# Optimization experiments

Measured on AMD Instinct MI355X. Metric: run time of the kernel, lower is better.

## Reference

```python
import jax, jax.numpy as jnp
import numpy as np

B, S, D = 2, 2048, 2048
H = 32
HD = D // H  # 64
EPS = 1e-4


def setup_inputs() -> dict:
    key = jax.random.key(0)
    ks = jax.random.split(key, 9)
    hidden_states = jax.random.normal(ks[0], (B, S, D), dtype=jnp.float32)
    # multiplicative causal mask
    attention_mask = jnp.tril(jnp.ones((S, S), dtype=jnp.float32))[None, None]
    scale = 0.02
    wq = jax.random.normal(ks[1], (D, D), dtype=jnp.float32) * scale
    wk = jax.random.normal(ks[2], (D, D), dtype=jnp.float32) * scale
    wv = jax.random.normal(ks[3], (D, D), dtype=jnp.float32) * scale
    wo = jax.random.normal(ks[4], (D, D), dtype=jnp.float32) * scale
    bq = jax.random.normal(ks[5], (D,), dtype=jnp.float32) * scale
    bk = jax.random.normal(ks[6], (D,), dtype=jnp.float32) * scale
    bv = jax.random.normal(ks[7], (D,), dtype=jnp.float32) * scale
    bo = jax.random.normal(ks[8], (D,), dtype=jnp.float32) * scale
    return {"hidden_states": hidden_states, "attention_mask": attention_mask,
            "wq": wq, "bq": bq, "wk": wk, "bk": bk, "wv": wv, "bv": bv,
            "wo": wo, "bo": bo}


def _split_heads(x):
    # [B, S, D] -> [B, H, S, HD]
    b, s, _ = x.shape
    return x.reshape(b, s, H, HD).transpose(0, 2, 1, 3)


def reference(hidden_states, attention_mask, wq, bq, wk, bk, wv, bv, wo, bo):
    scaling = HD ** -0.5
    q = (hidden_states @ wq.T + bq) * scaling
    k = hidden_states @ wk.T + bk
    v = hidden_states @ wv.T + bv
    q, k, v = _split_heads(q), _split_heads(k), _split_heads(v)
    # ELU+1 feature map, then sum-normalize over head dim
    q = jax.nn.elu(q) + 1.0
    k = jax.nn.elu(k) + 1.0
    q = q / (q.sum(-1, keepdims=True) + EPS)
    k = k / (k.sum(-1, keepdims=True) + EPS)
    # quadratic attention: [B, H, S, S]
    attn = jnp.einsum('bhsd,bhtd->bhst', q, k) * (HD ** -0.5)
    attn = attn * attention_mask  # multiplicative mask
    out = jnp.einsum('bhst,bhtd->bhsd', attn, v)  # [B, H, S, HD]
    out = out.transpose(0, 2, 1, 3).reshape(hidden_states.shape[0], -1, D)
    return out @ wo.T + bo
```

## Files before the change

kernel.cpp:

```cpp
#include <hip/hip_runtime.h>

typedef __bf16 bf16x8 __attribute__((ext_vector_type(8)));
typedef float f32x4 __attribute__((ext_vector_type(4)));

#define GLDS(g, l) __builtin_amdgcn_global_load_lds(                              \
    (const __attribute__((address_space(1))) void*)(g),                            \
    (__attribute__((address_space(3))) void*)(l), 16, 0, 0)

__device__ __forceinline__ unsigned short f2bf(float f) {
  unsigned int u = __builtin_bit_cast(unsigned int, f);
  u = (u + 0x7fffu + ((u >> 16) & 1u)) >> 16;
  return (unsigned short)u;
}
__device__ __forceinline__ float bf2f(unsigned short h) {
  unsigned int u = ((unsigned int)h) << 16;
  return __builtin_bit_cast(float, u);
}

__global__ __launch_bounds__(256) void cvt_f32_bf16(
    const float* __restrict__ in, unsigned short* __restrict__ out, int n4) {
  int i = blockIdx.x * 256 + threadIdx.x;
  if (i < n4) {
    float4 v = ((const float4*)in)[i];
    ushort4 o;
    o.x = f2bf(v.x); o.y = f2bf(v.y); o.z = f2bf(v.z); o.w = f2bf(v.w);
    ((ushort4*)out)[i] = o;
  }
}

__global__ __launch_bounds__(256) void cvt_w4(
    const float* __restrict__ w0, const float* __restrict__ w1,
    const float* __restrict__ w2, const float* __restrict__ w3,
    unsigned short* __restrict__ out) {
  const int y = blockIdx.y;
  const float* src = (y == 0) ? w0 : (y == 1) ? w1 : (y == 2) ? w2 : w3;
  const int i = blockIdx.x * 256 + threadIdx.x;
  float4 v = ((const float4*)src)[i];
  ushort4 o;
  o.x = f2bf(v.x); o.y = f2bf(v.y); o.z = f2bf(v.z); o.w = f2bf(v.w);
  ((ushort4*)(out + (size_t)y * 4194304))[i] = o;
}

__global__ __launch_bounds__(512, 2) void gemm256_qkv(
    const unsigned short* __restrict__ A, const unsigned short* __restrict__ Bw,
    const float* __restrict__ bq, const float* __restrict__ bk, const float* __restrict__ bv,
    unsigned short* __restrict__ oQ, unsigned short* __restrict__ oK,
    unsigned short* __restrict__ oV) {
  constexpr int K = 2048, NT = 32;
  __shared__ unsigned short lds[81920];
  const int tid = threadIdx.x, lane = tid & 63, wid = tid >> 6;
  const int wm = wid >> 2, wn = wid & 3;

  const int g0 = blockIdx.x;
  const int wg = (g0 & 7) * 48 + (g0 >> 3);
  const int l = wg % 96, chunk = wg / 96;
  const int bx = chunk * 6 + l / 16;
  const int by = l % 16;

  const int rloc = tid >> 3;
  const size_t gcoff = (size_t)(((lane & 7) ^ (lane >> 3)) << 3);
  const unsigned short* gA[4];
  const unsigned short* gB[4];
#pragma unroll
  for (int c = 0; c < 4; ++c) {
    gA[c] = A  + (size_t)(by * 256 + c * 64 + rloc) * K + gcoff;
    gB[c] = Bw + (size_t)(bx * 256 + c * 64 + rloc) * K + gcoff;
  }

#define ABu(b) ((b) * 16384)
#define BBu(b) (49152 + (b) * 16384)
#define STAGE_A(c, b) GLDS(gA[c], lds + ABu(b) + (c) * 4096 + wid * 512)
#define STAGE_B(c, b) GLDS(gB[c], lds + BBu(b) + (c) * 4096 + wid * 512)

  const int arow = (wm * 128 + (lane & 15)) * 64;
  const int brow = (wn * 64 + (lane & 15)) * 64;
  const int sw0 = (((lane >> 4)) ^ (lane & 7)) << 3;
  const int sw1 = ((4 + (lane >> 4)) ^ (lane & 7)) << 3;

  f32x4 acc[8][4] = {};

#pragma unroll
  for (int c = 0; c < 4; ++c) STAGE_A(c, 0);
#pragma unroll
  for (int c = 0; c < 4; ++c) gA[c] += 64;
#pragma unroll
  for (int c = 0; c < 4; ++c) STAGE_B(c, 0);
#pragma unroll
  for (int c = 0; c < 4; ++c) gB[c] += 64;
#pragma unroll
  for (int c = 0; c < 4; ++c) STAGE_A(c, 1);
#pragma unroll
  for (int c = 0; c < 4; ++c) gA[c] += 64;
  asm volatile("s_waitcnt vmcnt(4)" ::: "memory");
  __builtin_amdgcn_s_barrier();

  for (int t = 0; t < NT; ++t) {
    const int Ab = ABu(t % 3) + arow;
    const int Bb = BBu(t & 1) + brow;
    const int Asb = (t + 2) % 3, Bsb = (t + 1) & 1;
    const bool stA = (t + 2 < NT), stB = (t + 1 < NT);
    bf16x8 Af[4], Bf[4];

    if (stB) { STAGE_B(0, Bsb); STAGE_B(1, Bsb); }
#pragma unroll
    for (int n = 0; n < 4; ++n) Bf[n] = *(const bf16x8*)&lds[Bb + n * 1024 + sw0];
#pragma unroll
    for (int m = 0; m < 4; ++m) Af[m] = *(const bf16x8*)&lds[Ab + m * 1024 + sw0];
    __builtin_amdgcn_s_barrier();
    __builtin_amdgcn_s_setprio(1);
#pragma unroll
    for (int m = 0; m < 4; ++m)
#pragma unroll
      for (int n = 0; n < 4; ++n)
        acc[m][n] = __builtin_amdgcn_mfma_f32_16x16x32_bf16(Af[m], Bf[n], acc[m][n], 0, 0, 0);
    __builtin_amdgcn_s_setprio(0);
    __builtin_amdgcn_s_barrier();

    if (stB) {
      STAGE_B(2, Bsb); STAGE_B(3, Bsb);
#pragma unroll
      for (int c = 0; c < 4; ++c) gB[c] += 64;
    }
#pragma unroll
    for (int m = 0; m < 4; ++m) Af[m] = *(const bf16x8*)&lds[Ab + (m + 4) * 1024 + sw0];
    __builtin_amdgcn_s_barrier();
    __builtin_amdgcn_s_setprio(1);
#pragma unroll
    for (int m = 0; m < 4; ++m)
#pragma unroll
      for (int n = 0; n < 4; ++n)
        acc[m + 4][n] = __builtin_amdgcn_mfma_f32_16x16x32_bf16(Af[m], Bf[n], acc[m + 4][n], 0, 0, 0);
    __builtin_amdgcn_s_setprio(0);
    __builtin_amdgcn_s_barrier();

    if (stA) { STAGE_A(0, Asb); STAGE_A(1, Asb); }
#pragma unroll
    for (int n = 0; n < 4; ++n) Bf[n] = *(const bf16x8*)&lds[Bb + n * 1024 + sw1];
#pragma unroll
    for (int m = 0; m < 4; ++m) Af[m] = *(const bf16x8*)&lds[Ab + m * 1024 + sw1];
    __builtin_amdgcn_s_barrier();
    __builtin_amdgcn_s_setprio(1);
#pragma unroll
    for (int m = 0; m < 4; ++m)
#pragma unroll
      for (int n = 0; n < 4; ++n)
        acc[m][n] = __builtin_amdgcn_mfma_f32_16x16x32_bf16(Af[m], Bf[n], acc[m][n], 0, 0, 0);
    __builtin_amdgcn_s_setprio(0);
    __builtin_amdgcn_s_barrier();

    if (stA) {
      STAGE_A(2, Asb); STAGE_A(3, Asb);
#pragma unroll
      for (int c = 0; c < 4; ++c) gA[c] += 64;
    }
#pragma unroll
    for (int m = 0; m < 4; ++m) Af[m] = *(const bf16x8*)&lds[Ab + (m + 4) * 1024 + sw1];
    __builtin_amdgcn_s_barrier();
    __builtin_amdgcn_s_setprio(1);
#pragma unroll
    for (int m = 0; m < 4; ++m)
#pragma unroll
      for (int n = 0; n < 4; ++n)
        acc[m + 4][n] = __builtin_amdgcn_mfma_f32_16x16x32_bf16(Af[m], Bf[n], acc[m + 4][n], 0, 0, 0);
    __builtin_amdgcn_s_setprio(0);
    if (stA)      asm volatile("s_waitcnt vmcnt(4)" ::: "memory");
    else if (stB) asm volatile("s_waitcnt vmcnt(0)" ::: "memory");
    __builtin_amdgcn_s_barrier();
  }

  const int head = bx * 4 + wn;
  const int type = head >> 5;
  const int h = head & 31;
  const float* bias = (type == 0) ? bq : (type == 1) ? bk : bv;
  unsigned short* dst = (type == 0) ? oQ : (type == 1) ? oK : oV;
  float bv4[4];
#pragma unroll
  for (int n = 0; n < 4; ++n) bv4[n] = bias[h * 64 + n * 16 + (lane & 15)];
#pragma unroll
  for (int m = 0; m < 8; ++m) {
#pragma unroll
    for (int r = 0; r < 4; ++r) {
      const int row = by * 256 + wm * 128 + m * 16 + ((lane >> 4) << 2) + r;
      const int bb = row >> 11, s = row & 2047;
      float e[4];
      float loc = 0.f;
#pragma unroll
      for (int n = 0; n < 4; ++n) {
        float v = acc[m][n][r] + bv4[n];
        if (type == 0) v *= 0.125f;
        if (type < 2) v = (v > 0.f) ? (v + 1.f) : __expf(v);
        e[n] = v; loc += v;
      }
      if (type < 2) {
#pragma unroll
        for (int off = 1; off < 16; off <<= 1) loc += __shfl_xor(loc, off, 64);
        const float inv = 1.f / (loc + 1e-4f);
#pragma unroll
        for (int n = 0; n < 4; ++n) e[n] *= inv;
      }
      const size_t base = ((size_t)((bb << 5) + h) * 2048 + s) * 64;
#pragma unroll
      for (int n = 0; n < 4; ++n) dst[base + n * 16 + (lane & 15)] = f2bf(e[n]);
    }
  }
#undef ABu
#undef BBu
#undef STAGE_A
#undef STAGE_B
}

__global__ __launch_bounds__(512, 2) void gemm128_wo(
    const unsigned short* __restrict__ A, const unsigned short* __restrict__ Bw,
    const float* __restrict__ b0, float* __restrict__ C) {
  constexpr int K = 2048, NT = 32;
  __shared__ unsigned short lds[73728];
  const int tid = threadIdx.x, lane = tid & 63, wid = tid >> 6;
  const int wm = wid >> 2, wn = wid & 3;

  constexpr int NWG = 256, CPX = NWG >> 3;
  const int g0 = blockIdx.x;
  const int wg = (g0 & 7) * CPX + (g0 >> 3);
  const int l = wg % 32;
  const int chunk = wg / 32;
  const int bx = chunk * 2 + l / 16;
  const int by = l % 16 + ((chunk >= 4) ? 0 : 0);
  const int bx2 = (chunk % 4) * 2 + l / 16;
  const int by2 = (chunk / 4) * 16 + l % 16;
  (void)bx; (void)by;

  const int rloc = wid * 8 + (lane >> 3);
  const size_t gcoff = (size_t)(((lane & 7) ^ (lane >> 3)) << 3);
  const unsigned short* gA[2];
  const unsigned short* gB[4];
#pragma unroll
  for (int c = 0; c < 2; ++c) gA[c] = A + (size_t)(by2 * 128 + c * 64 + rloc) * K + gcoff;
#pragma unroll
  for (int c = 0; c < 4; ++c) gB[c] = Bw + (size_t)(bx2 * 256 + c * 64 + rloc) * K + gcoff;

  int aoff[4][2], boff[4][2];
#pragma unroll
  for (int m = 0; m < 4; ++m)
#pragma unroll
    for (int kk = 0; kk < 2; ++kk) {
      aoff[m][kk] = (wm * 64 + m * 16 + (lane & 15)) * 64 +
                    ((((kk << 2) + (lane >> 4)) ^ (lane & 7)) << 3);
      boff[m][kk] = (wn * 64 + m * 16 + (lane & 15)) * 64 +
                    ((((kk << 2) + (lane >> 4)) ^ (lane & 7)) << 3);
    }

  f32x4 acc[4][4] = {};

#define AB(b) ((b) * 8192)
#define BB(b) (24576 + (b) * 16384)
#define STAGE_A(c, b) GLDS(gA[c], lds + AB(b) + (c) * 4096 + wid * 512)
#define STAGE_B(c, b) GLDS(gB[c], lds + BB(b) + (c) * 4096 + wid * 512)

  STAGE_A(0, 0); STAGE_A(1, 0); STAGE_B(0, 0); STAGE_B(1, 0); STAGE_B(2, 0); STAGE_B(3, 0);
#pragma unroll
  for (int c = 0; c < 2; ++c) gA[c] += 64;
#pragma unroll
  for (int c = 0; c < 4; ++c) gB[c] += 64;
  STAGE_A(0, 1); STAGE_A(1, 1); STAGE_B(0, 1); STAGE_B(1, 1); STAGE_B(2, 1); STAGE_B(3, 1);
#pragma unroll
  for (int c = 0; c < 2; ++c) gA[c] += 64;
#pragma unroll
  for (int c = 0; c < 4; ++c) gB[c] += 64;
  asm volatile("s_waitcnt vmcnt(6)" ::: "memory");
  __builtin_amdgcn_s_barrier();

  for (int t = 0; t < NT; ++t) {
    const int b = t % 3;
    const int sb = (t + 2) % 3;
    const bool doStage = (t + 2 < NT);

    if (doStage) { STAGE_A(0, sb); STAGE_A(1, sb); STAGE_B(0, sb); STAGE_B(1, sb); }
    bf16x8 af[4], bfr[4];
#pragma unroll
    for (int m = 0; m < 4; ++m) af[m] = *(const bf16x8*)&lds[AB(b) + aoff[m][0]];
#pragma unroll
    for (int n = 0; n < 4; ++n) bfr[n] = *(const bf16x8*)&lds[BB(b) + boff[n][0]];
    __builtin_amdgcn_s_barrier();
    __builtin_amdgcn_s_setprio(1);
#pragma unroll
    for (int m = 0; m < 4; ++m)
#pragma unroll
      for (int n = 0; n < 4; ++n)
        acc[m][n] = __builtin_amdgcn_mfma_f32_16x16x32_bf16(af[m], bfr[n], acc[m][n], 0, 0, 0);
    __builtin_amdgcn_s_setprio(0);
    __builtin_amdgcn_s_barrier();

    if (doStage) { STAGE_B(2, sb); STAGE_B(3, sb); }
#pragma unroll
    for (int c = 0; c < 2; ++c) gA[c] += 64;
#pragma unroll
    for (int c = 0; c < 4; ++c) gB[c] += 64;
#pragma unroll
    for (int m = 0; m < 4; ++m) af[m] = *(const bf16x8*)&lds[AB(b) + aoff[m][1]];
#pragma unroll
    for (int n = 0; n < 4; ++n) bfr[n] = *(const bf16x8*)&lds[BB(b) + boff[n][1]];
    __builtin_amdgcn_s_barrier();
    __builtin_amdgcn_s_setprio(1);
#pragma unroll
    for (int m = 0; m < 4; ++m)
#pragma unroll
      for (int n = 0; n < 4; ++n)
        acc[m][n] = __builtin_amdgcn_mfma_f32_16x16x32_bf16(af[m], bfr[n], acc[m][n], 0, 0, 0);
    __builtin_amdgcn_s_setprio(0);
    if (t < NT - 1) {
      if (doStage) asm volatile("s_waitcnt vmcnt(6)" ::: "memory");
      else         asm volatile("s_waitcnt vmcnt(0)" ::: "memory");
    }
    __builtin_amdgcn_s_barrier();
  }

#pragma unroll
  for (int n = 0; n < 4; ++n) {
    const int col = bx2 * 256 + wn * 64 + n * 16 + (lane & 15);
    const float bv_ = b0[col];
#pragma unroll
    for (int m = 0; m < 4; ++m) {
      const int row0 = by2 * 128 + wm * 64 + m * 16 + ((lane >> 4) << 2);
#pragma unroll
      for (int r = 0; r < 4; ++r)
        C[(size_t)(row0 + r) * 2048 + col] = acc[m][n][r] + bv_;
    }
  }
#undef AB
#undef BB
#undef STAGE_A
#undef STAGE_B
}

__global__ __launch_bounds__(256) void chunk_state(
    const unsigned short* __restrict__ Kn, const unsigned short* __restrict__ Vn,
    unsigned short* __restrict__ stT) {
  __shared__ unsigned short Kt[64 * 72];
  __shared__ unsigned short Vt[64 * 72];
  const int c = blockIdx.x, bh = blockIdx.y;
  const int tid = threadIdx.x, lane = tid & 63, wid = tid >> 6;
  const size_t base = (size_t)bh * 2048 * 64 + (size_t)c * 64 * 64;
#pragma unroll
  for (int i = 0; i < 16; ++i) {
    const int ii = i * 256 + tid;
    const int t = ii >> 6, d = ii & 63;
    Kt[d * 72 + t] = Kn[base + ii];
    Vt[d * 72 + t] = Vn[base + ii];
  }
  __syncthreads();
  f32x4 acc[4] = {};
#pragma unroll
  for (int ks = 0; ks < 2; ++ks) {
    const int ko = ks * 32 + (lane >> 4) * 8;
    bf16x8 a = *(const bf16x8*)&Vt[(wid * 16 + (lane & 15)) * 72 + ko];
#pragma unroll
    for (int ej = 0; ej < 4; ++ej) {
      bf16x8 bb = *(const bf16x8*)&Kt[(ej * 16 + (lane & 15)) * 72 + ko];
      acc[ej] = __builtin_amdgcn_mfma_f32_16x16x32_bf16(a, bb, acc[ej], 0, 0, 0);
    }
  }
  const size_t obase = ((size_t)bh * 32 + c) * 4096;
#pragma unroll
  for (int ej = 0; ej < 4; ++ej) {
    const int e = ej * 16 + (lane & 15);
    const int d0 = wid * 16 + ((lane >> 4) << 2);
#pragma unroll
    for (int r = 0; r < 4; ++r)
      stT[obase + (size_t)(d0 + r) * 64 + e] = f2bf(acc[ej][r]);
  }
}

__global__ __launch_bounds__(256) void prefix_state(
    const unsigned short* __restrict__ stT, unsigned short* __restrict__ cumT) {
  const int g = blockIdx.x * 256 + threadIdx.x;
  const int bh = g >> 12, e = g & 4095;
  float run = 0.f;
  for (int c = 0; c < 32; ++c) {
    const size_t idx = (((size_t)bh * 32 + c) << 12) + e;
    const float v = bf2f(stT[idx]);
    cumT[idx] = f2bf(run);
    run += v;
  }
}

__global__ __launch_bounds__(256) void attn_intra(
    const unsigned short* __restrict__ Qn, const unsigned short* __restrict__ Kn,
    const unsigned short* __restrict__ Vn, const unsigned short* __restrict__ cumT,
    unsigned short* __restrict__ aout) {
  __shared__ unsigned short Qs[64 * 72];
  __shared__ unsigned short Ks[64 * 72];
  __shared__ unsigned short Vt[64 * 72];
  __shared__ unsigned short St[64 * 72];
  __shared__ unsigned short Ps[64 * 72];
  const int c = blockIdx.x, bh = blockIdx.y;
  const int tid = threadIdx.x, lane = tid & 63, wid = tid >> 6;
  const size_t base = (size_t)bh * 2048 * 64 + (size_t)c * 64 * 64;
  const size_t sbase = ((size_t)bh * 32 + c) * 4096;
#pragma unroll
  for (int i = 0; i < 16; ++i) {
    const int ii = i * 256 + tid;
    const int t = ii >> 6, d = ii & 63;
    Qs[t * 72 + d] = Qn[base + ii];
    Ks[t * 72 + d] = Kn[base + ii];
    Vt[d * 72 + t] = Vn[base + ii];
    St[t * 72 + d] = cumT[sbase + ii];
  }
  __syncthreads();
  f32x4 sacc[4] = {};
#pragma unroll
  for (int ks = 0; ks < 2; ++ks) {
    const int ko = ks * 32 + (lane >> 4) * 8;
    bf16x8 a = *(const bf16x8*)&Qs[(wid * 16 + (lane & 15)) * 72 + ko];
#pragma unroll
    for (int tj = 0; tj < 4; ++tj) {
      bf16x8 bb = *(const bf16x8*)&Ks[(tj * 16 + (lane & 15)) * 72 + ko];
      sacc[tj] = __builtin_amdgcn_mfma_f32_16x16x32_bf16(a, bb, sacc[tj], 0, 0, 0);
    }
  }
#pragma unroll
  for (int tj = 0; tj < 4; ++tj) {
    const int t = tj * 16 + (lane & 15);
    const int s0 = wid * 16 + ((lane >> 4) << 2);
#pragma unroll
    for (int r = 0; r < 4; ++r) {
      const float v = (t <= s0 + r) ? sacc[tj][r] : 0.f;
      Ps[(s0 + r) * 72 + t] = f2bf(v);
    }
  }
  __syncthreads();
  f32x4 oacc[4] = {};
#pragma unroll
  for (int ks = 0; ks < 2; ++ks) {
    const int ko = ks * 32 + (lane >> 4) * 8;
    bf16x8 a = *(const bf16x8*)&Ps[(wid * 16 + (lane & 15)) * 72 + ko];
    bf16x8 a2 = *(const bf16x8*)&Qs[(wid * 16 + (lane & 15)) * 72 + ko];
#pragma unroll
    for (int dj = 0; dj < 4; ++dj) {
      bf16x8 bv_ = *(const bf16x8*)&Vt[(dj * 16 + (lane & 15)) * 72 + ko];
      oacc[dj] = __builtin_amdgcn_mfma_f32_16x16x32_bf16(a, bv_, oacc[dj], 0, 0, 0);
      bf16x8 bs_ = *(const bf16x8*)&St[(dj * 16 + (lane & 15)) * 72 + ko];
      oacc[dj] = __builtin_amdgcn_mfma_f32_16x16x32_bf16(a2, bs_, oacc[dj], 0, 0, 0);
    }
  }
  const int b = bh >> 5, h = bh & 31;
#pragma unroll
  for (int dj = 0; dj < 4; ++dj) {
    const int d = dj * 16 + (lane & 15);
    const int s0 = wid * 16 + ((lane >> 4) << 2);
#pragma unroll
    for (int r = 0; r < 4; ++r) {
      const size_t row = (size_t)(b * 2048 + c * 64 + s0 + r);
      aout[row * 2048 + h * 64 + d] = f2bf(0.125f * oacc[dj][r]);
    }
  }
}

extern "C" void kernel_launch(void* const* d_in, const int* in_sizes, int n_in,
                              void* d_out, int out_size, void* d_ws, size_t ws_size,
                              hipStream_t stream) {
  const float* hs = (const float*)d_in[0];
  const float* wq = (const float*)d_in[2];
  const float* bq = (const float*)d_in[3];
  const float* wk = (const float*)d_in[4];
  const float* bk = (const float*)d_in[5];
  const float* wv = (const float*)d_in[6];
  const float* bv = (const float*)d_in[7];
  const float* wo = (const float*)d_in[8];
  const float* bo = (const float*)d_in[9];
  float* out = (float*)d_out;
  char* ws = (char*)d_ws;

  unsigned short* hs_bf   = (unsigned short*)(ws);
  unsigned short* wall_bf = (unsigned short*)(ws + 16777216);
  unsigned short* Qn      = (unsigned short*)(ws + 50331648);
  unsigned short* Kn      = (unsigned short*)(ws + 67108864);
  unsigned short* Vn      = (unsigned short*)(ws + 83886080);
  unsigned short* stT     = (unsigned short*)(ws + 100663296);
  unsigned short* cumT    = (unsigned short*)(ws + 117440512);
  unsigned short* aout    = (unsigned short*)(ws + 134217728);

  cvt_f32_bf16<<<8192, 256, 0, stream>>>(hs, hs_bf, 2097152);
  cvt_w4<<<dim3(4096, 4), 256, 0, stream>>>(wq, wk, wv, wo, wall_bf);

  gemm256_qkv<<<384, 512, 0, stream>>>(hs_bf, wall_bf, bq, bk, bv, Qn, Kn, Vn);

  chunk_state<<<dim3(32, 64), 256, 0, stream>>>(Kn, Vn, stT);
  prefix_state<<<1024, 256, 0, stream>>>(stT, cumT);
  attn_intra<<<dim3(32, 64), 256, 0, stream>>>(Qn, Kn, Vn, cumT, aout);

  gemm128_wo<<<256, 512, 0, stream>>>(aout, wall_bf + 12582912, bo, out);
}
```

Measured before the change: 229.4 us.

## Retile QKV GEMM to 256x384 tiles with 256 workgroups and 2-stage buffering

```diff
diff --git a/kernel.cpp b/kernel.cpp
--- a/kernel.cpp
+++ b/kernel.cpp
@@ -41,7 +41,7 @@
   ((ushort4*)(out + (size_t)y * 4194304))[i] = o;
 }
 
-__global__ __launch_bounds__(512, 2) void gemm256_qkv(
+__global__ __launch_bounds__(512, 2) void gemm384_qkv(
     const unsigned short* __restrict__ A, const unsigned short* __restrict__ Bw,
     const float* __restrict__ bq, const float* __restrict__ bk, const float* __restrict__ bv,
     unsigned short* __restrict__ oQ, unsigned short* __restrict__ oK,
@@ -49,158 +49,141 @@
   constexpr int K = 2048, NT = 32;
   __shared__ unsigned short lds[81920];
   const int tid = threadIdx.x, lane = tid & 63, wid = tid >> 6;
-  const int wm = wid >> 2, wn = wid & 3;
+  const int wm = wid >> 1, wn = wid & 1;
 
   const int g0 = blockIdx.x;
-  const int wg = (g0 & 7) * 48 + (g0 >> 3);
-  const int l = wg % 96, chunk = wg / 96;
-  const int bx = chunk * 6 + l / 16;
-  const int by = l % 16;
+  const int wg = (g0 & 7) * 32 + (g0 >> 3);
+  const int chunk = wg >> 5, l = wg & 31;
+  const int bx = (chunk & 3) * 4 + (l >> 3);
+  const int by = (chunk >> 2) * 8 + (l & 7);
 
   const int rloc = tid >> 3;
   const size_t gcoff = (size_t)(((lane & 7) ^ (lane >> 3)) << 3);
-  const unsigned short* gA[4];
-  const unsigned short* gB[4];
-#pragma unroll
-  for (int c = 0; c < 4; ++c) {
-    gA[c] = A  + (size_t)(by * 256 + c * 64 + rloc) * K + gcoff;
-    gB[c] = Bw + (size_t)(bx * 256 + c * 64 + rloc) * K + gcoff;
-  }
+  const unsigned short* gA = A  + (size_t)(by * 256 + rloc) * K + gcoff;
+  const unsigned short* gB = Bw + (size_t)(bx * 384 + rloc) * K + gcoff;
 
 #define ABu(b) ((b) * 16384)
-#define BBu(b) (49152 + (b) * 16384)
-#define STAGE_A(c, b) GLDS(gA[c], lds + ABu(b) + (c) * 4096 + wid * 512)
-#define STAGE_B(c, b) GLDS(gB[c], lds + BBu(b) + (c) * 4096 + wid * 512)
-
-  const int arow = (wm * 128 + (lane & 15)) * 64;
-  const int brow = (wn * 64 + (lane & 15)) * 64;
+#define BBu(b) (32768 + (b) * 24576)
+#define STAGE_A(c, b) GLDS(gA + (size_t)(c) * 64 * K, lds + ABu(b) + (c) * 4096 + wid * 512)
+#define STAGE_B(c, b) GLDS(gB + (size_t)(c) * 64 * K, lds + BBu(b) + (c) * 4096 + wid * 512)
+
+  const int arow = (wm * 64 + (lane & 15)) * 64;
+  const int brow = (wn * 192 + (lane & 15)) * 64;
   const int sw0 = (((lane >> 4)) ^ (lane & 7)) << 3;
   const int sw1 = ((4 + (lane >> 4)) ^ (lane & 7)) << 3;
 
-  f32x4 acc[8][4] = {};
-
-#pragma unroll
-  for (int c = 0; c < 4; ++c) STAGE_A(c, 0);
-#pragma unroll
-  for (int c = 0; c < 4; ++c) gA[c] += 64;
-#pragma unroll
-  for (int c = 0; c < 4; ++c) STAGE_B(c, 0);
-#pragma unroll
-  for (int c = 0; c < 4; ++c) gB[c] += 64;
-#pragma unroll
-  for (int c = 0; c < 4; ++c) STAGE_A(c, 1);
-#pragma unroll
-  for (int c = 0; c < 4; ++c) gA[c] += 64;
-  asm volatile("s_waitcnt vmcnt(4)" ::: "memory");
+  f32x4 acc[4][12] = {};
+
+  STAGE_A(0, 0); STAGE_A(1, 0); STAGE_A(2, 0); STAGE_A(3, 0);
+  STAGE_B(0, 0); STAGE_B(1, 0); STAGE_B(2, 0); STAGE_B(3, 0); STAGE_B(4, 0); STAGE_B(5, 0);
+  gA += 64; gB += 64;
+  asm volatile("s_waitcnt vmcnt(0)" ::: "memory");
   __builtin_amdgcn_s_barrier();
 
   for (int t = 0; t < NT; ++t) {
-    const int Ab = ABu(t % 3) + arow;
+    const int Ab = ABu(t & 1) + arow;
     const int Bb = BBu(t & 1) + brow;
-    const int Asb = (t + 2) % 3, Bsb = (t + 1) & 1;
-    const bool stA = (t + 2 < NT), stB = (t + 1 < NT);
-    bf16x8 Af[4], Bf[4];
-
-    if (stB) { STAGE_B(0, Bsb); STAGE_B(1, Bsb); }
-#pragma unroll
-    for (int n = 0; n < 4; ++n) Bf[n] = *(const bf16x8*)&lds[Bb + n * 1024 + sw0];
+    const int sb = (t + 1) & 1;
+    const bool st = (t + 1 < NT);
+    bf16x8 Af[4], Bf[6];
+
+    if (st) { STAGE_B(0, sb); STAGE_B(1, sb); STAGE_B(2, sb); }
 #pragma unroll
     for (int m = 0; m < 4; ++m) Af[m] = *(const bf16x8*)&lds[Ab + m * 1024 + sw0];
-    __builtin_amdgcn_s_barrier();
-    __builtin_amdgcn_s_setprio(1);
-#pragma unroll
-    for (int m = 0; m < 4; ++m)
-#pragma unroll
-      for (int n = 0; n < 4; ++n)
+#pragma unroll
+    for (int n = 0; n < 6; ++n) Bf[n] = *(const bf16x8*)&lds[Bb + n * 1024 + sw0];
+    __builtin_amdgcn_s_barrier();
+    __builtin_amdgcn_s_setprio(1);
+#pragma unroll
+    for (int m = 0; m < 4; ++m)
+#pragma unroll
+      for (int n = 0; n < 6; ++n)
         acc[m][n] = __builtin_amdgcn_mfma_f32_16x16x32_bf16(Af[m], Bf[n], acc[m][n], 0, 0, 0);
     __builtin_amdgcn_s_setprio(0);
     __builtin_amdgcn_s_barrier();
 
-    if (stB) {
-      STAGE_B(2, Bsb); STAGE_B(3, Bsb);
-#pragma unroll
-      for (int c = 0; c < 4; ++c) gB[c] += 64;
-    }
-#pragma unroll
-    for (int m = 0; m < 4; ++m) Af[m] = *(const bf16x8*)&lds[Ab + (m + 4) * 1024 + sw0];
-    __builtin_amdgcn_s_barrier();
-    __builtin_amdgcn_s_setprio(1);
-#pragma unroll
-    for (int m = 0; m < 4; ++m)
-#pragma unroll
-      for (int n = 0; n < 4; ++n)
-        acc[m + 4][n] = __builtin_amdgcn_mfma_f32_16x16x32_bf16(Af[m], Bf[n], acc[m + 4][n], 0, 0, 0);
-    __builtin_amdgcn_s_setprio(0);
-    __builtin_amdgcn_s_barrier();
-
-    if (stA) { STAGE_A(0, Asb); STAGE_A(1, Asb); }
-#pragma unroll
-    for (int n = 0; n < 4; ++n) Bf[n] = *(const bf16x8*)&lds[Bb + n * 1024 + sw1];
+    if (st) { STAGE_B(3, sb); STAGE_B(4, sb); STAGE_B(5, sb); }
+#pragma unroll
+    for (int n = 0; n < 6; ++n) Bf[n] = *(const bf16x8*)&lds[Bb + (n + 6) * 1024 + sw0];
+    __builtin_amdgcn_s_barrier();
+    __builtin_amdgcn_s_setprio(1);
+#pragma unroll
+    for (int m = 0; m < 4; ++m)
+#pragma unroll
+      for (int n = 0; n < 6; ++n)
+        acc[m][n + 6] = __builtin_amdgcn_mfma_f32_16x16x32_bf16(Af[m], Bf[n], acc[m][n + 6], 0, 0, 0);
+    __builtin_amdgcn_s_setprio(0);
+    __builtin_amdgcn_s_barrier();
+
+    if (st) { STAGE_A(0, sb); STAGE_A(1, sb); STAGE_A(2, sb); STAGE_A(3, sb); }
 #pragma unroll
     for (int m = 0; m < 4; ++m) Af[m] = *(const bf16x8*)&lds[Ab + m * 1024 + sw1];
-    __builtin_amdgcn_s_barrier();
-    __builtin_amdgcn_s_setprio(1);
-#pragma unroll
-    for (int m = 0; m < 4; ++m)
-#pragma unroll
-      for (int n = 0; n < 4; ++n)
+#pragma unroll
+    for (int n = 0; n < 6; ++n) Bf[n] = *(const bf16x8*)&lds[Bb + n * 1024 + sw1];
+    __builtin_amdgcn_s_barrier();
+    __builtin_amdgcn_s_setprio(1);
+#pragma unroll
+    for (int m = 0; m < 4; ++m)
+#pragma unroll
+      for (int n = 0; n < 6; ++n)
         acc[m][n] = __builtin_amdgcn_mfma_f32_16x16x32_bf16(Af[m], Bf[n], acc[m][n], 0, 0, 0);
     __builtin_amdgcn_s_setprio(0);
     __builtin_amdgcn_s_barrier();
 
-    if (stA) {
-      STAGE_A(2, Asb); STAGE_A(3, Asb);
-#pragma unroll
-      for (int c = 0; c < 4; ++c) gA[c] += 64;
-    }
-#pragma unroll
-    for (int m = 0; m < 4; ++m) Af[m] = *(const bf16x8*)&lds[Ab + (m + 4) * 1024 + sw1];
-    __builtin_amdgcn_s_barrier();
-    __builtin_amdgcn_s_setprio(1);
-#pragma unroll
-    for (int m = 0; m < 4; ++m)
-#pragma unroll
-      for (int n = 0; n < 4; ++n)
-        acc[m + 4][n] = __builtin_amdgcn_mfma_f32_16x16x32_bf16(Af[m], Bf[n], acc[m + 4][n], 0, 0, 0);
-    __builtin_amdgcn_s_setprio(0);
-    if (stA)      asm volatile("s_waitcnt vmcnt(4)" ::: "memory");
-    else if (stB) asm volatile("s_waitcnt vmcnt(0)" ::: "memory");
-    __builtin_amdgcn_s_barrier();
-  }
-
-  const int head = bx * 4 + wn;
-  const int type = head >> 5;
-  const int h = head & 31;
-  const float* bias = (type == 0) ? bq : (type == 1) ? bk : bv;
-  unsigned short* dst = (type == 0) ? oQ : (type == 1) ? oK : oV;
-  float bv4[4];
-#pragma unroll
-  for (int n = 0; n < 4; ++n) bv4[n] = bias[h * 64 + n * 16 + (lane & 15)];
-#pragma unroll
-  for (int m = 0; m < 8; ++m) {
-#pragma unroll
-    for (int r = 0; r < 4; ++r) {
-      const int row = by * 256 + wm * 128 + m * 16 + ((lane >> 4) << 2) + r;
-      const int bb = row >> 11, s = row & 2047;
-      float e[4];
-      float loc = 0.f;
-#pragma unroll
-      for (int n = 0; n < 4; ++n) {
-        float v = acc[m][n][r] + bv4[n];
-        if (type == 0) v *= 0.125f;
-        if (type < 2) v = (v > 0.f) ? (v + 1.f) : __expf(v);
-        e[n] = v; loc += v;
+#pragma unroll
+    for (int n = 0; n < 6; ++n) Bf[n] = *(const bf16x8*)&lds[Bb + (n + 6) * 1024 + sw1];
+    __builtin_amdgcn_s_barrier();
+    __builtin_amdgcn_s_setprio(1);
+#pragma unroll
+    for (int m = 0; m < 4; ++m)
+#pragma unroll
+      for (int n = 0; n < 6; ++n)
+        acc[m][n + 6] = __builtin_amdgcn_mfma_f32_16x16x32_bf16(Af[m], Bf[n], acc[m][n + 6], 0, 0, 0);
+    __builtin_amdgcn_s_setprio(0);
+    if (st) {
+      gA += 64; gB += 64;
+      asm volatile("s_waitcnt vmcnt(0)" ::: "memory");
+    }
+    __builtin_amdgcn_s_barrier();
+  }
+
+  const int head0 = bx * 6 + wn * 3;
+#pragma unroll
+  for (int g = 0; g < 3; ++g) {
+    const int head = head0 + g;
+    const int type = head >> 5;
+    const int h = head & 31;
+    const float* bias = (type == 0) ? bq : (type == 1) ? bk : bv;
+    unsigned short* dst = (type == 0) ? oQ : (type == 1) ? oK : oV;
+    float bv4[4];
+#pragma unroll
+    for (int j = 0; j < 4; ++j) bv4[j] = bias[h * 64 + j * 16 + (lane & 15)];
+#pragma unroll
+    for (int m = 0; m < 4; ++m) {
+#pragma unroll
+      for (int r = 0; r < 4; ++r) {
+        const int row = by * 256 + wm * 64 + m * 16 + ((lane >> 4) << 2) + r;
+        const int bb = row >> 11, s = row & 2047;
+        float e[4];
+        float loc = 0.f;
+#pragma unroll
+        for (int j = 0; j < 4; ++j) {
+          float v = acc[m][g * 4 + j][r] + bv4[j];
+          if (type == 0) v *= 0.125f;
+          if (type < 2) v = (v > 0.f) ? (v + 1.f) : __expf(v);
+          e[j] = v; loc += v;
+        }
+        if (type < 2) {
+#pragma unroll
+          for (int off = 1; off < 16; off <<= 1) loc += __shfl_xor(loc, off, 64);
+          const float inv = 1.f / (loc + 1e-4f);
+#pragma unroll
+          for (int j = 0; j < 4; ++j) e[j] *= inv;
+        }
+        const size_t base = ((size_t)((bb << 5) + h) * 2048 + s) * 64;
+#pragma unroll
+        for (int j = 0; j < 4; ++j) dst[base + j * 16 + (lane & 15)] = f2bf(e[j]);
       }
-      if (type < 2) {
-#pragma unroll
-        for (int off = 1; off < 16; off <<= 1) loc += __shfl_xor(loc, off, 64);
-        const float inv = 1.f / (loc + 1e-4f);
-#pragma unroll
-        for (int n = 0; n < 4; ++n) e[n] *= inv;
-      }
-      const size_t base = ((size_t)((bb << 5) + h) * 2048 + s) * 64;
-#pragma unroll
-      for (int n = 0; n < 4; ++n) dst[base + n * 16 + (lane & 15)] = f2bf(e[n]);
     }
   }
 #undef ABu
@@ -217,16 +200,12 @@
   const int tid = threadIdx.x, lane = tid & 63, wid = tid >> 6;
   const int wm = wid >> 2, wn = wid & 3;
 
-  constexpr int NWG = 256, CPX = NWG >> 3;
   const int g0 = blockIdx.x;
-  const int wg = (g0 & 7) * CPX + (g0 >> 3);
+  const int wg = (g0 & 7) * 32 + (g0 >> 3);
   const int l = wg % 32;
   const int chunk = wg / 32;
-  const int bx = chunk * 2 + l / 16;
-  const int by = l % 16 + ((chunk >= 4) ? 0 : 0);
   const int bx2 = (chunk % 4) * 2 + l / 16;
   const int by2 = (chunk / 4) * 16 + l % 16;
-  (void)bx; (void)by;
 
   const int rloc = wid * 8 + (lane >> 3);
   const size_t gcoff = (size_t)(((lane & 7) ^ (lane >> 3)) << 3);
@@ -481,7 +460,7 @@
   cvt_f32_bf16<<<8192, 256, 0, stream>>>(hs, hs_bf, 2097152);
   cvt_w4<<<dim3(4096, 4), 256, 0, stream>>>(wq, wk, wv, wo, wall_bf);
 
-  gemm256_qkv<<<384, 512, 0, stream>>>(hs_bf, wall_bf, bq, bk, bv, Qn, Kn, Vn);
+  gemm384_qkv<<<256, 512, 0, stream>>>(hs_bf, wall_bf, bq, bk, bv, Qn, Kn, Vn);
 
   chunk_state<<<dim3(32, 64), 256, 0, stream>>>(Kn, Vn, stT);
   prefix_state<<<1024, 256, 0, stream>>>(stT, cumT);
```

Result: faster. 200.6 us (-12.6%).
